# Optimization experiments

Hardware: AMD Instinct MI355X
Metric: run time of the kernel (lower is better)

## Reference

```python
import jax, jax.numpy as jnp
import numpy as np

B, N, K = 4, 1500, 30
NODE_F, EDGE_F, H = 1024, 128, 128
L, NUM_RBF, NUM_POS, NHEADS = 4, 16, 16, 4
DH = H // NHEADS
LN_EPS = 1e-6


def setup_inputs() -> dict:
    key = jax.random.key(0)
    ks = jax.random.split(key, 16)
    g = lambda k, shp: jax.random.normal(k, shp, jnp.float32) / np.sqrt(shp[-2] if len(shp) > 1 else 1.0)
    return {
        'X': jax.random.normal(ks[0], (B, N, 3), jnp.float32) * 10.0,
        'V': jax.random.normal(ks[1], (B, N, NODE_F), jnp.float32),
        'mask': jnp.ones((B, N), jnp.float32),
        'W_v': g(ks[2], (NODE_F, H)), 'b_v': jnp.zeros((H,), jnp.float32),
        'W_e': g(ks[3], (EDGE_F, H)), 'b_e': jnp.zeros((H,), jnp.float32),
        'W_edge': g(ks[4], (NUM_POS + NUM_RBF, EDGE_F)),
        'ln_e_g': jnp.ones((EDGE_F,), jnp.float32), 'ln_e_b': jnp.zeros((EDGE_F,), jnp.float32),
        'Wq': g(ks[5], (L, H, H)), 'Wk': g(ks[6], (L, 2 * H, H)),
        'Wv_a': g(ks[7], (L, 2 * H, H)), 'Wo': g(ks[8], (L, H, H)),
        'ln1_g': jnp.ones((L, H), jnp.float32), 'ln1_b': jnp.zeros((L, H), jnp.float32),
        'ln2_g': jnp.ones((L, H), jnp.float32), 'ln2_b': jnp.zeros((L, H), jnp.float32),
        'W_ff1': g(ks[9], (L, H, 4 * H)), 'b_ff1': jnp.zeros((L, 4 * H), jnp.float32),
        'W_ff2': g(ks[10], (L, 4 * H, H)), 'b_ff2': jnp.zeros((L, H), jnp.float32),
        'W_out': g(ks[11], (H, 1)), 'b_out': jnp.zeros((1,), jnp.float32),
    }


def _layer_norm(x, gamma, beta):
    mu = jnp.mean(x, -1, keepdims=True)
    var = jnp.var(x, -1, keepdims=True)
    return gamma * (x - mu) / jnp.sqrt(var + LN_EPS) + beta


def _gather_nodes(nodes, idx):
    # nodes [B,N,C], idx [B,N,K] -> [B,N,K,C]
    return jax.vmap(lambda n, i: n[i])(nodes, idx)


def reference(X, V, mask, W_v, b_v, W_e, b_e, W_edge, ln_e_g, ln_e_b, Wq, Wk, Wv_a, Wo,
              ln1_g, ln1_b, ln2_g, ln2_b, W_ff1, b_ff1, W_ff2, b_ff2, W_out, b_out):
    # ---- EdgeFeatures: masked pairwise distances + kNN topk ----
    mask2 = mask[:, :, None] * mask[:, None, :]            # [B,N,N]
    dX = X[:, :, None, :] - X[:, None, :, :]               # [B,N,N,3]
    D = mask2 * jnp.sqrt(jnp.sum(dX * dX, -1) + 1e-6)
    D_adj = D + (1.0 - mask2) * jnp.max(D, -1, keepdims=True)
    negD, E_idx = jax.lax.top_k(-D_adj, K)                 # k smallest distances
    D_nb = -negD                                           # [B,N,K]
    # RBF of neighbor distances
    mu = jnp.linspace(0.0, 20.0, NUM_RBF)
    sigma = 20.0 / NUM_RBF
    rbf = jnp.exp(-(((D_nb[..., None] - mu) / sigma) ** 2))  # [B,N,K,NUM_RBF]
    # sinusoidal relative positional encodings of neighbor offsets
    ii = jnp.arange(N, dtype=jnp.float32)[None, :, None]
    d_rel = (E_idx.astype(jnp.float32) - ii)[..., None]
    freq = jnp.exp(jnp.arange(0, NUM_POS, 2, dtype=jnp.float32) * (-np.log(10000.0) / NUM_POS))
    ang = d_rel * freq
    pos = jnp.concatenate([jnp.cos(ang), jnp.sin(ang)], -1)  # [B,N,K,NUM_POS]
    E = jnp.concatenate([pos, rbf], -1) @ W_edge
    E = _layer_norm(E, ln_e_g, ln_e_b)                     # [B,N,K,EDGE_F]
    # ---- node / edge embeddings ----
    h_V = V @ W_v + b_v                                    # [B,N,H]
    h_E = E @ W_e + b_e                                    # [B,N,K,H]
    mask_attend = mask[:, :, None] * _gather_nodes(mask[..., None], E_idx)[..., 0]  # [B,N,K]
    neg_inf = jnp.float32(np.finfo(np.float32).min)
    # ---- encoder layers ----
    for l in range(L):
        h_EV = jnp.concatenate([h_E, _gather_nodes(h_V, E_idx)], -1)  # [B,N,K,2H]
        Q = (h_V @ Wq[l]).reshape(B, N, NHEADS, DH)
        Kh = (h_EV @ Wk[l]).reshape(B, N, K, NHEADS, DH)
        Vh = (h_EV @ Wv_a[l]).reshape(B, N, K, NHEADS, DH)
        logits = jnp.einsum('bnhd,bnkhd->bnhk', Q, Kh) / np.sqrt(DH)
        m = mask_attend[:, :, None, :]                     # [B,N,1,K]
        attend = jax.nn.softmax(jnp.where(m > 0, logits, neg_inf), -1) * m
        upd = jnp.einsum('bnhk,bnkhd->bnhd', attend, Vh).reshape(B, N, H) @ Wo[l]
        h_V = _layer_norm(h_V + upd, ln1_g[l], ln1_b[l])
        dh = jax.nn.relu(h_V @ W_ff1[l] + b_ff1[l]) @ W_ff2[l] + b_ff2[l]
        h_V = _layer_norm(h_V + dh, ln2_g[l], ln2_b[l])
        h_V = mask[..., None] * h_V
    return (h_V @ W_out + b_out)[..., 0]                   # [B,N] logits
```

## Files before the change

### kernel.cpp

```cpp
#include <hip/hip_runtime.h>
#include <hip/hip_bf16.h>
#include <math.h>

#define NB 4
#define NN 1500
#define KNB 30
#define H 128
#define NHEADS 4
#define FFH 512
#define NODE_FEAT 1024
#define NROWS (NB*NN)
#define LN_EPS 1e-6f

#define P_F32_STRIDE 384
#define P_BF16_STRIDE 768

typedef __attribute__((ext_vector_type(8))) short s8v;
typedef __attribute__((ext_vector_type(4))) float f4v;

__device__ __forceinline__ float bf_lo(unsigned u){ union{unsigned i; float f;} v; v.i = u<<16; return v.f; }
__device__ __forceinline__ float bf_hi(unsigned u){ union{unsigned i; float f;} v; v.i = u & 0xffff0000u; return v.f; }

__device__ __forceinline__ void find_bucket30(
    const unsigned* hist, int base0, int t, int lane, int wave,
    int* wsum, int* res)
{
    int h[16], s = 0;
    const uint4* hp = (const uint4*)&hist[(t & 127) * 16];
    int sh = (t >> 7) << 4;
    uint4 w[4] = {hp[0], hp[1], hp[2], hp[3]};
#pragma unroll
    for (int i = 0; i < 4; i++) {
        h[i*4+0] = (w[i].x >> sh) & 0xffff;
        h[i*4+1] = (w[i].y >> sh) & 0xffff;
        h[i*4+2] = (w[i].z >> sh) & 0xffff;
        h[i*4+3] = (w[i].w >> sh) & 0xffff;
        s += h[i*4+0] + h[i*4+1] + h[i*4+2] + h[i*4+3];
    }
    int inc = s;
#pragma unroll
    for (int off = 1; off < 64; off <<= 1) {
        int o = __shfl_up(inc, off, 64);
        if (lane >= off) inc += o;
    }
    if (lane == 63) wsum[wave] = inc;
    __syncthreads();
    int base = base0 + inc - s;
    for (int w2 = 0; w2 < wave; w2++) base += wsum[w2];
    if (base < KNB && base + s >= KNB) {
        int running = base;
#pragma unroll
        for (int i = 0; i < 16; i++) {
            if (running < KNB && running + h[i] >= KNB) { res[0] = (t<<4)|i; res[1] = running; break; }
            running += h[i];
        }
    }
    __syncthreads();
}

__global__ __launch_bounds__(256) void topk_kernel(
    const float* __restrict__ X, const float* __restrict__ mask,
    int* __restrict__ E_idx, float* __restrict__ D_nb)
{
    int row = blockIdx.x;
    int b = row / NN;
    int t = threadIdx.x;
    int wave = t >> 6, lane = t & 63;
    __shared__ float d_adj[NN];
    __shared__ unsigned hist[2048];
    __shared__ float redw[4];
    __shared__ int   wsum[4];
    __shared__ int   res[2];
    __shared__ int   cand[64];
    __shared__ int   ncand;

    float xi0 = X[row*3+0], xi1 = X[row*3+1], xi2 = X[row*3+2];
    float mi = mask[row];

    float dr[6], m2r[6];
    float lmax = -1e30f;
#pragma unroll
    for (int q = 0; q < 6; q++) {
        int j = t + q*256;
        float d = 0.f, m2 = 0.f;
        if (j < NN) {
            float dx = xi0 - X[(b*NN+j)*3+0];
            float dy = xi1 - X[(b*NN+j)*3+1];
            float dz = xi2 - X[(b*NN+j)*3+2];
            d  = sqrtf(dx*dx + dy*dy + dz*dz + 1e-6f);
            m2 = mi * mask[b*NN+j];
            lmax = fmaxf(lmax, m2*d);
        }
        dr[q] = d; m2r[q] = m2;
    }
    for (int q = t; q < 2048; q += 256) hist[q] = 0;
#pragma unroll
    for (int off = 32; off > 0; off >>= 1)
        lmax = fmaxf(lmax, __shfl_xor(lmax, off, 64));
    if (lane == 0) redw[wave] = lmax;
    if (t == 0) ncand = 0;
    __syncthreads();
    float rowmax = fmaxf(fmaxf(redw[0], redw[1]), fmaxf(redw[2], redw[3]));

    unsigned kreg[6];
#pragma unroll
    for (int q = 0; q < 6; q++) {
        int j = t + q*256;
        if (j < NN) {
            float dv = m2r[q]*dr[q] + (1.0f - m2r[q])*rowmax;
            d_adj[j] = dv;
            unsigned key = __float_as_uint(dv);
            kreg[q] = key;
            unsigned bkt = key >> 20;
            atomicAdd(&hist[bkt & 2047], 1u << ((bkt >> 11) << 4));
        } else kreg[q] = 0xFFFFFFFFu;
    }
    __syncthreads();

    find_bucket30(hist, 0, t, lane, wave, wsum, res);
    int B1 = res[0], nb1 = res[1];

    for (int q = t; q < 2048; q += 256) hist[q] = 0;
    __syncthreads();
#pragma unroll
    for (int q = 0; q < 6; q++) {
        if ((kreg[q] >> 20) == (unsigned)B1) {
            unsigned bkt = (kreg[q] >> 8) & 0xFFF;
            atomicAdd(&hist[bkt & 2047], 1u << ((bkt >> 11) << 4));
        }
    }
    __syncthreads();

    find_bucket30(hist, nb1, t, lane, wave, wsum, res);
    unsigned Bfull = ((unsigned)B1 << 12) | (unsigned)res[0];

#pragma unroll
    for (int q = 0; q < 6; q++) {
        if ((kreg[q] >> 8) <= Bfull) {
            int slot = atomicAdd(&ncand, 1);
            if (slot < 64) cand[slot] = t + q*256;
        }
    }
    __syncthreads();

    if (wave == 0) {
        int nc = min(ncand, 64);
        if (lane < nc) {
            int j = cand[lane];
            float v = d_adj[j];
            int rank = 0;
            for (int m = 0; m < nc; m++) {
                int jm = cand[m];
                float vm = d_adj[jm];
                rank += (vm < v || (vm == v && jm < j)) ? 1 : 0;
            }
            if (rank < KNB) {
                E_idx[row*KNB + rank] = j;
                D_nb[row*KNB + rank]  = v;
            }
        }
    }
}

__global__ __launch_bounds__(256) void wprep_edge_kernel(
    const float* __restrict__ W_edge, __hip_bfloat16* __restrict__ W_edge_t)
{
    int tid = blockIdx.x*256 + threadIdx.x;
    int n = tid >> 5, k = tid & 31;
    W_edge_t[tid] = __float2bfloat16(W_edge[k*H + n]);
}

__global__ __launch_bounds__(256) void edge_kernel(
    const int* __restrict__ E_idx, const float* __restrict__ D_nb,
    const __hip_bfloat16* __restrict__ W_edge_t, const float* __restrict__ ln_g,
    const float* __restrict__ ln_b, __hip_bfloat16* __restrict__ E_ln)
{
    int g0 = blockIdx.x * 2;
    int t = threadIdx.x;
    int wave = t >> 6, lane = t & 63, lm = lane & 15, lq = lane >> 4;
    __shared__ __hip_bfloat16 Es[64*136];

    int row = wave*16 + lm;
    int rr = row < 60 ? row : 59;
    int node = g0 + (rr >= KNB ? 1 : 0);
    int e = node*KNB + (rr >= KNB ? rr - KNB : rr);
    float drel = (float)(E_idx[e] - (node % NN));
    float dnb  = D_nb[e];

    const float FR[8] = {1.f, 0.31622776601683794f, 0.1f, 0.031622776601683794f,
                         0.01f, 0.0031622776601683794f, 0.001f, 0.00031622776601683794f};
    union { s8v v; __hip_bfloat16 h[8]; } af;
    if (lq == 0) {
#pragma unroll
        for (int j = 0; j < 8; j++) af.h[j] = __float2bfloat16(cosf(drel*FR[j]));
    } else if (lq == 1) {
#pragma unroll
        for (int j = 0; j < 8; j++) af.h[j] = __float2bfloat16(sinf(drel*FR[j]));
    } else {
        int f0 = (lq-2)*8;
#pragma unroll
        for (int j = 0; j < 8; j++) {
            float mu = (20.0f/15.0f) * (float)(f0+j);
            float z = (dnb - mu) * 0.8f;
            af.h[j] = __float2bfloat16(expf(-z*z));
        }
    }

    f4v acc[8];
#pragma unroll
    for (int nt = 0; nt < 8; nt++) {
        s8v bf = *(const s8v*)&W_edge_t[(nt*16+lm)*32 + lq*8];
        f4v z = {0.f,0.f,0.f,0.f};
        acc[nt] = __builtin_amdgcn_mfma_f32_16x16x32_bf16(af.v, bf, z, 0,0,0);
    }

    float gv[8], bv[8];
#pragma unroll
    for (int nt = 0; nt < 8; nt++) { gv[nt] = ln_g[nt*16+lm]; bv[nt] = ln_b[nt*16+lm]; }
#pragma unroll
    for (int r = 0; r < 4; r++) {
        float sm = 0.f, sq = 0.f;
#pragma unroll
        for (int nt = 0; nt < 8; nt++) { float x = acc[nt][r]; sm += x; sq += x*x; }
#pragma unroll
        for (int m = 1; m < 16; m <<= 1) {
            sm += __shfl_xor(sm, m, 64);
            sq += __shfl_xor(sq, m, 64);
        }
        float mu = sm * (1.0f/H);
        float rs = rsqrtf(sq*(1.0f/H) - mu*mu + LN_EPS);
        int erow = wave*16 + lq*4 + r;
#pragma unroll
        for (int nt = 0; nt < 8; nt++)
            Es[erow*136 + nt*16 + lm] =
                __float2bfloat16(gv[nt]*(acc[nt][r]-mu)*rs + bv[nt]);
    }
    __syncthreads();

    __hip_bfloat16* dst = E_ln + (size_t)g0*KNB*H;
    for (int q = t; q < 960; q += 256) {
        int r = q >> 4, c8 = (q & 15) * 8;
        *(s8v*)&dst[r*H + c8] = *(const s8v*)&Es[r*136 + c8];
    }
}

__global__ __launch_bounds__(256) void wprep_v_kernel(
    const float* __restrict__ W_v, __hip_bfloat16* __restrict__ Wv_t)
{
    int tid = blockIdx.x*256 + threadIdx.x;
    int n = tid & 127, k = tid >> 7;
    Wv_t[(size_t)n*NODE_FEAT + k] = __float2bfloat16(W_v[k*H + n]);
}

__global__ __launch_bounds__(128) void wprep_kv_kernel(
    const float* __restrict__ W_e, const float* __restrict__ b_e,
    const float* __restrict__ Wk, const float* __restrict__ Wv,
    float* __restrict__ Wkv_f, float* __restrict__ bias_kv)
{
    int l = blockIdx.x >> 8;
    int n = blockIdx.x & 255;
    int t = threadIdx.x;
    int col = n & 127;
    const float* W = (n < 128) ? (Wk + l*2*H*H) : (Wv + l*2*H*H);
    __shared__ float wcol[128];
    wcol[t] = W[t*H + col];
    __syncthreads();
    float a = 0.f;
    for (int c = 0; c < H; c += 4) {
        float4 we = *(const float4*)&W_e[t*H + c];
        a += we.x*wcol[c] + we.y*wcol[c+1] + we.z*wcol[c+2] + we.w*wcol[c+3];
    }
    Wkv_f[(size_t)(l*256 + n)*H + t] = a;
    if (t == 0) {
        float bsum = 0.f;
        for (int c = 0; c < H; c++) bsum += b_e[c]*wcol[c];
        bias_kv[l*256 + n] = bsum;
    }
}

__global__ __launch_bounds__(128) void wprep_qp_kernel(
    const float* __restrict__ Wq, const float* __restrict__ Wkv_f,
    __hip_bfloat16* __restrict__ Wn_t)
{
    int l = blockIdx.x >> 9;
    int m = blockIdx.x & 511;
    int h = m >> 7, e = m & 127;
    int c = threadIdx.x;
    __shared__ float wek[32];
    if (c < 32) wek[c] = Wkv_f[(size_t)(l*256 + h*32 + c)*H + e];
    __syncthreads();
    const float* wq = Wq + (size_t)l*16384 + c*128 + h*32;
    float a = 0.f;
#pragma unroll
    for (int d = 0; d < 32; d++) a += wq[d]*wek[d];
    Wn_t[(size_t)(l*896 + 128 + m)*H + c] = __float2bfloat16(a);
}

__global__ __launch_bounds__(128) void wprep_op_kernel(
    const float* __restrict__ Wo, const float* __restrict__ Wkv_f,
    __hip_bfloat16* __restrict__ WoU_t)
{
    int l = blockIdx.x / 640;
    int kk = blockIdx.x - l*640;
    int n = threadIdx.x;
    __shared__ float wev[32];
    if (kk < 512) {
        int h = kk >> 7;
        int e = kk & 127;
        if (n < 32) wev[n] = Wkv_f[(size_t)(l*256 + 128 + h*32 + n)*H + e];
    }
    __syncthreads();
    float v;
    if (kk < 512) {
        int h = kk >> 7;
        float a = 0.f;
#pragma unroll
        for (int d = 0; d < 32; d++)
            a += wev[d]*Wo[(size_t)l*16384 + (h*32+d)*128 + n];
        v = a;
    } else {
        v = Wo[(size_t)l*16384 + (kk-512)*128 + n];
    }
    WoU_t[((size_t)l*128 + n)*640 + kk] = __float2bfloat16(v);
}

__global__ __launch_bounds__(256) void wprep_post_kernel(
    const float* __restrict__ Wf1, const float* __restrict__ Wf2,
    const float* __restrict__ Wq, const float* __restrict__ Wk,
    const float* __restrict__ Wv,
    __hip_bfloat16* __restrict__ Wf1_t, __hip_bfloat16* __restrict__ Wf2_t,
    __hip_bfloat16* __restrict__ Wn_t)
{
    int id = blockIdx.x*256 + threadIdx.x;
    int l = id / 180224;
    int r = id - l*180224;
    float v; __hip_bfloat16* dst;
    if (r < 65536) {
        int n = r >> 7, k = r & 127;
        v = Wf1[(size_t)l*65536 + k*512 + n];
        dst = Wf1_t + (size_t)l*65536 + r;
    } else if (r < 131072) {
        int rr = r - 65536;
        int n = rr >> 9, k = rr & 511;
        v = Wf2[(size_t)l*65536 + k*128 + n];
        dst = Wf2_t + (size_t)l*65536 + rr;
    } else if (r < 147456) {
        int rr = r - 131072;
        int n = rr >> 7, k = rr & 127;
        v = Wq[(size_t)l*16384 + k*128 + n];
        dst = Wn_t + (size_t)l*114688 + rr;
    } else {
        int rr = r - 147456;
        int n = rr >> 7, k = rr & 127;
        v = (n < 128) ? Wk[(size_t)l*32768 + (128+k)*128 + n]
                      : Wv[(size_t)l*32768 + (128+k)*128 + (n-128)];
        dst = Wn_t + (size_t)l*114688 + 81920 + rr;
    }
    *dst = __float2bfloat16(v);
}

__global__ __launch_bounds__(256) void hv_init_kernel(
    const float* __restrict__ V, const __hip_bfloat16* __restrict__ Wv_t,
    const float* __restrict__ b_v, float* __restrict__ hv,
    const __hip_bfloat16* __restrict__ Wn_t, float* __restrict__ P,
    __hip_bfloat16* __restrict__ PKV)
{
    int row0 = blockIdx.x * 16;
    int t = threadIdx.x;
    int wave = t >> 6, lane = t & 63, lm = lane & 15, lq = lane >> 4;
    __shared__ __hip_bfloat16 Vs[16*1032];
    __shared__ __hip_bfloat16 zs[16*136];

    for (int q = t; q < 4096; q += 256) {
        int r = q >> 8, c4 = (q & 255) * 4;
        float4 v4 = *(const float4*)&V[(size_t)(row0+r)*NODE_FEAT + c4];
        __hip_bfloat16* d = &Vs[r*1032 + c4];
        d[0] = __float2bfloat16(v4.x);
        d[1] = __float2bfloat16(v4.y);
        d[2] = __float2bfloat16(v4.z);
        d[3] = __float2bfloat16(v4.w);
    }
    __syncthreads();

#pragma unroll
    for (int ntl = 0; ntl < 2; ntl++) {
        int nt = wave*2 + ntl;
        f4v acc = {0.f,0.f,0.f,0.f};
        for (int ks = 0; ks < 32; ks++) {
            s8v af = *(const s8v*)&Vs[lm*1032 + ks*32 + lq*8];
            s8v bf = *(const s8v*)&Wv_t[(size_t)(nt*16+lm)*NODE_FEAT + ks*32 + lq*8];
            acc = __builtin_amdgcn_mfma_f32_16x16x32_bf16(af, bf, acc, 0,0,0);
        }
        int cc = nt*16 + lm;
        float b = b_v[cc];
#pragma unroll
        for (int r = 0; r < 4; r++) {
            int rr = lq*4 + r;
            float v = acc[r] + b;
            hv[(size_t)(row0+rr)*H + cc] = v;
            zs[rr*136+cc] = __float2bfloat16(v);
        }
    }
    __syncthreads();

    __hip_bfloat16* Pb = (__hip_bfloat16*)P;
    for (int ntl = 0; ntl < 14; ntl++) {
        int nt = wave*14 + ntl;
        f4v acc = {0.f,0.f,0.f,0.f};
#pragma unroll
        for (int ks = 0; ks < 4; ks++) {
            s8v af = *(const s8v*)&zs[lm*136 + ks*32 + lq*8];
            s8v bf = *(const s8v*)&Wn_t[(size_t)(nt*16+lm)*H + ks*32 + lq*8];
            acc = __builtin_amdgcn_mfma_f32_16x16x32_bf16(af, bf, acc, 0,0,0);
        }
        int cc = nt*16 + lm;
#pragma unroll
        for (int r = 0; r < 4; r++) {
            int rr = row0 + lq*4 + r;
            if (cc < 128)
                P[(size_t)rr*P_F32_STRIDE + cc] = acc[r];
            else if (cc < 640)
                Pb[(size_t)rr*P_BF16_STRIDE + 128 + cc] = __float2bfloat16(acc[r]);
            else
                PKV[(size_t)rr*256 + (cc-640)] = __float2bfloat16(acc[r]);
        }
    }
}

__global__ __launch_bounds__(256) void attn_kernel(
    const __hip_bfloat16* __restrict__ E_ln, const float* __restrict__ biasv,
    float* __restrict__ P, const __hip_bfloat16* __restrict__ PKV,
    const int* __restrict__ E_idx, const float* __restrict__ mask)
{
    int g0 = blockIdx.x * 2;
    int t = threadIdx.x;
    int wave = t >> 6, lane = t & 63, lm = lane & 15, lq = lane >> 4;
    __shared__ __hip_bfloat16 Es[60*136];
    __shared__ float Qs[2*128];
    __shared__ __hip_bfloat16 Qp[2*512];
    __shared__ float att_s[2*128];
    __shared__ float ssum[8];
    __shared__ float mv_s[60];
    __shared__ int   nbr[60];

    const __hip_bfloat16* hebase = E_ln + (size_t)g0*KNB*H;
    for (int q = t; q < 960; q += 256) {
        int r = q >> 4, c8 = (q & 15) * 8;
        *(s8v*)&Es[r*136 + c8] = *(const s8v*)&hebase[r*H + c8];
    }
    const __hip_bfloat16* Pb = (const __hip_bfloat16*)P;
    if (t < 128) {
        int node = t >> 6, c8 = (t & 63)*8;
        *(s8v*)&Qp[node*512 + c8] = *(const s8v*)&Pb[(size_t)(g0+node)*P_BF16_STRIDE + 256 + c8];
    }
    {
        int node = t >> 7, c = t & 127;
        Qs[t] = P[(size_t)(g0+node)*P_F32_STRIDE + c];
    }
    if (t < 60) {
        int gn = g0 + t/30;
        int b = gn / NN;
        int idx = E_idx[gn*KNB + (t%30)];
        nbr[t]  = b*NN + idx;
        mv_s[t] = mask[gn] * mask[b*NN + idx];
    }
    __syncthreads();

    if (t < 240) {
        int node = t/120, tt = t%120, h = tt/30, kk = tt%30;
        const uint4* ep = (const uint4*)&Es[(node*30+kk)*136];
        const uint4* qp = (const uint4*)&Qp[node*512 + h*128];
        float a = 0.f;
#pragma unroll
        for (int j = 0; j < 16; j++) {
            uint4 e4 = ep[j], q4 = qp[j];
            a += bf_lo(e4.x)*bf_lo(q4.x) + bf_hi(e4.x)*bf_hi(q4.x);
            a += bf_lo(e4.y)*bf_lo(q4.y) + bf_hi(e4.y)*bf_hi(q4.y);
            a += bf_lo(e4.z)*bf_lo(q4.z) + bf_hi(e4.z)*bf_hi(q4.z);
            a += bf_lo(e4.w)*bf_lo(q4.w) + bf_hi(e4.w)*bf_hi(q4.w);
        }
        const uint4* kb = (const uint4*)(PKV + (size_t)nbr[node*30+kk]*256 + h*32);
        const float* q = &Qs[node*128 + h*32];
#pragma unroll
        for (int j = 0; j < 4; j++) {
            uint4 u = kb[j];
            const float* q8 = q + j*8;
            a += q8[0]*bf_lo(u.x) + q8[1]*bf_hi(u.x)
               + q8[2]*bf_lo(u.y) + q8[3]*bf_hi(u.y)
               + q8[4]*bf_lo(u.z) + q8[5]*bf_hi(u.z)
               + q8[6]*bf_lo(u.w) + q8[7]*bf_hi(u.w);
        }
        int r = node*30 + kk;
        att_s[node*128 + h*32 + kk] =
            (mv_s[r] > 0.f) ? a*0.17677669529663687f : -3.4028235e38f;
    }
    __syncthreads();

    if (wave < 2) {
        int node = wave, h = lq, j = lm;
        float* ap = &att_s[node*128 + h*32];
        const float* mp = &mv_s[node*30];
        float a0 = ap[j];
        float a1 = (j+16 < KNB) ? ap[j+16] : -3.4028235e38f;
        float mx = fmaxf(a0, a1);
#pragma unroll
        for (int m = 1; m < 16; m <<= 1) mx = fmaxf(mx, __shfl_xor(mx, m, 64));
        float e0 = __expf(a0 - mx);
        float e1 = (j+16 < KNB) ? __expf(a1 - mx) : 0.f;
        float s = e0 + e1;
#pragma unroll
        for (int m = 1; m < 16; m <<= 1) s += __shfl_xor(s, m, 64);
        float inv = 1.0f / s;
        float w0 = e0 * inv * mp[j];
        float w1 = (j+16 < KNB) ? e1 * inv * mp[j+16] : 0.f;
        ap[j] = w0;
        if (j+16 < KNB) ap[j+16] = w1;
        float ss = w0 + w1;
#pragma unroll
        for (int m = 1; m < 16; m <<= 1) ss += __shfl_xor(ss, m, 64);
        if (j == 0) ssum[node*4 + h] = ss;
    }
    __syncthreads();

    {
        int node = t >> 7, c = t & 127, h = c >> 5;
        __hip_bfloat16* Ub = (__hip_bfloat16*)P + (size_t)(g0+node)*P_BF16_STRIDE;
        const float* ap = &att_s[node*128];
        const int* nb = &nbr[node*30];

        float u = ssum[node*4 + h] * biasv[c];
        const float* ah = ap + h*32;
        for (int k = 0; k < KNB; k++)
            u += ah[k] * __bfloat162float(PKV[(size_t)nb[k]*256 + 128 + c]);
        Ub[512 + c] = __float2bfloat16(u);

        float s0 = 0.f, s1 = 0.f, s2 = 0.f, s3 = 0.f;
        for (int k = 0; k < KNB; k++) {
            float e = __bfloat162float(Es[(node*30+k)*136 + c]);
            s0 += ap[k]      * e;
            s1 += ap[32+k]   * e;
            s2 += ap[64+k]   * e;
            s3 += ap[96+k]   * e;
        }
        Ub[c]       = __float2bfloat16(s0);
        Ub[128 + c] = __float2bfloat16(s1);
        Ub[256 + c] = __float2bfloat16(s2);
        Ub[384 + c] = __float2bfloat16(s3);
    }
}

__global__ __launch_bounds__(512) void post_kernel(
    float* __restrict__ hv, float* __restrict__ P,
    __hip_bfloat16* __restrict__ PKV, const float* __restrict__ mask,
    const __hip_bfloat16* __restrict__ WoU_t,
    const float* __restrict__ ln1g, const float* __restrict__ ln1b,
    const float* __restrict__ ln2g, const float* __restrict__ ln2b,
    const __hip_bfloat16* __restrict__ Wf1_t, const float* __restrict__ bf1,
    const __hip_bfloat16* __restrict__ Wf2_t, const float* __restrict__ bf2,
    const __hip_bfloat16* __restrict__ Wn_t)
{
    int row0 = blockIdx.x * 16;
    int t = threadIdx.x;
    int wave = t >> 6, lane = t & 63, lm = lane & 15, lq = lane >> 4;

    __shared__ __hip_bfloat16 Aus[16*648];
    __shared__ float xs[16*132];
    __shared__ __hip_bfloat16 ys[16*136];
    __shared__ __hip_bfloat16 t1[16*520];
    __shared__ __hip_bfloat16 zs[16*136];
    __shared__ float ps[512], pq[512];
    __shared__ float mu_s[16], rs_s[16];

    const __hip_bfloat16* Pbc = (const __hip_bfloat16*)P;
    for (int q = t; q < 1280; q += 512) {
        int r = q/80, c8 = (q%80)*8;
        *(s8v*)&Aus[r*648 + c8] = *(const s8v*)&Pbc[(size_t)(row0+r)*P_BF16_STRIDE + c8];
    }
    __syncthreads();

    {
        int nt = wave;
        f4v acc = {0.f,0.f,0.f,0.f};
        for (int ks = 0; ks < 20; ks++) {
            s8v af = *(const s8v*)&Aus[lm*648 + ks*32 + lq*8];
            s8v bf = *(const s8v*)&WoU_t[(size_t)(nt*16+lm)*640 + ks*32 + lq*8];
            acc = __builtin_amdgcn_mfma_f32_16x16x32_bf16(af, bf, acc, 0,0,0);
        }
        int cc = nt*16 + lm;
#pragma unroll
        for (int r = 0; r < 4; r++) {
            int rr = lq*4 + r;
            xs[rr*132+cc] = hv[(size_t)(row0+rr)*128 + cc] + acc[r];
        }
    }
    __syncthreads();

    {
        int r = t >> 5, s = t & 31;
        float4 a = *(const float4*)&xs[r*132 + s*4];
        ps[t] = a.x+a.y+a.z+a.w;
        pq[t] = a.x*a.x+a.y*a.y+a.z*a.z+a.w*a.w;
    }
    __syncthreads();
    if (t < 16) {
        float sm = 0.f, sq = 0.f;
        for (int s = 0; s < 32; s++) { sm += ps[t*32+s]; sq += pq[t*32+s]; }
        float mu = sm*(1.0f/H);
        mu_s[t] = mu;
        rs_s[t] = rsqrtf(sq*(1.0f/H) - mu*mu + LN_EPS);
    }
    __syncthreads();
    for (int q = t; q < 2048; q += 512) {
        int r = q >> 7, c = q & 127;
        float v = ln1g[c]*(xs[r*132+c]-mu_s[r])*rs_s[r] + ln1b[c];
        xs[r*132+c] = v;
        ys[r*136+c] = __float2bfloat16(v);
    }
    __syncthreads();

    for (int ntl = 0; ntl < 4; ntl++) {
        int nt = wave*4 + ntl;
        f4v acc = {0.f,0.f,0.f,0.f};
#pragma unroll
        for (int ks = 0; ks < 4; ks++) {
            s8v af = *(const s8v*)&ys[lm*136 + ks*32 + lq*8];
            s8v bf = *(const s8v*)&Wf1_t[(size_t)(nt*16+lm)*128 + ks*32 + lq*8];
            acc = __builtin_amdgcn_mfma_f32_16x16x32_bf16(af, bf, acc, 0,0,0);
        }
        int cc = nt*16 + lm;
        float b = bf1[cc];
#pragma unroll
        for (int r = 0; r < 4; r++)
            t1[(lq*4+r)*520 + cc] = __float2bfloat16(fmaxf(acc[r]+b, 0.f));
    }
    __syncthreads();

    {
        int nt = wave;
        f4v acc = {0.f,0.f,0.f,0.f};
#pragma unroll
        for (int ks = 0; ks < 16; ks++) {
            s8v af = *(const s8v*)&t1[lm*520 + ks*32 + lq*8];
            s8v bf = *(const s8v*)&Wf2_t[(size_t)(nt*16+lm)*512 + ks*32 + lq*8];
            acc = __builtin_amdgcn_mfma_f32_16x16x32_bf16(af, bf, acc, 0,0,0);
        }
        int cc = nt*16 + lm;
        float b = bf2[cc];
#pragma unroll
        for (int r = 0; r < 4; r++) {
            int rr = lq*4 + r;
            xs[rr*132+cc] = xs[rr*132+cc] + acc[r] + b;
        }
    }
    __syncthreads();

    {
        int r = t >> 5, s = t & 31;
        float4 a = *(const float4*)&xs[r*132 + s*4];
        ps[t] = a.x+a.y+a.z+a.w;
        pq[t] = a.x*a.x+a.y*a.y+a.z*a.z+a.w*a.w;
    }
    __syncthreads();
    if (t < 16) {
        float sm = 0.f, sq = 0.f;
        for (int s = 0; s < 32; s++) { sm += ps[t*32+s]; sq += pq[t*32+s]; }
        float mu = sm*(1.0f/H);
        mu_s[t] = mu;
        rs_s[t] = rsqrtf(sq*(1.0f/H) - mu*mu + LN_EPS);
    }
    __syncthreads();
    for (int q = t; q < 2048; q += 512) {
        int r = q >> 7, c = q & 127;
        float v = mask[row0+r]*(ln2g[c]*(xs[r*132+c]-mu_s[r])*rs_s[r] + ln2b[c]);
        hv[(size_t)(row0+r)*128 + c] = v;
        zs[r*136+c] = __float2bfloat16(v);
    }
    __syncthreads();

    if (Wn_t) {
        __hip_bfloat16* Pbw = (__hip_bfloat16*)P;
        for (int ntl = 0; ntl < 7; ntl++) {
            int nt = wave*7 + ntl;
            f4v acc = {0.f,0.f,0.f,0.f};
#pragma unroll
            for (int ks = 0; ks < 4; ks++) {
                s8v af = *(const s8v*)&zs[lm*136 + ks*32 + lq*8];
                s8v bf = *(const s8v*)&Wn_t[(size_t)(nt*16+lm)*128 + ks*32 + lq*8];
                acc = __builtin_amdgcn_mfma_f32_16x16x32_bf16(af, bf, acc, 0,0,0);
            }
            int cc = nt*16 + lm;
#pragma unroll
            for (int r = 0; r < 4; r++) {
                int rr = row0 + lq*4 + r;
                if (cc < 128)
                    P[(size_t)rr*P_F32_STRIDE + cc] = acc[r];
                else if (cc < 640)
                    Pbw[(size_t)rr*P_BF16_STRIDE + 128 + cc] = __float2bfloat16(acc[r]);
                else
                    PKV[(size_t)rr*256 + (cc-640)] = __float2bfloat16(acc[r]);
            }
        }
    }
}

__global__ __launch_bounds__(64) void out_kernel(
    const float* __restrict__ hv, const float* __restrict__ W_out,
    const float* __restrict__ b_out, float* __restrict__ out)
{
    int row = blockIdx.x;
    int t = threadIdx.x;
    float a = hv[row*H+t]*W_out[t] + hv[row*H+t+64]*W_out[t+64];
#pragma unroll
    for (int s = 32; s > 0; s >>= 1) a += __shfl_down(a, s, 64);
    if (t == 0) out[row] = a + b_out[0];
}

extern "C" void kernel_launch(void* const* d_in, const int* in_sizes, int n_in,
                              void* d_out, int out_size, void* d_ws, size_t ws_size,
                              hipStream_t stream)
{
    const float* X      = (const float*)d_in[0];
    const float* V      = (const float*)d_in[1];
    const float* mask   = (const float*)d_in[2];
    const float* W_v    = (const float*)d_in[3];
    const float* b_v    = (const float*)d_in[4];
    const float* W_e    = (const float*)d_in[5];
    const float* b_e    = (const float*)d_in[6];
    const float* W_edge = (const float*)d_in[7];
    const float* ln_e_g = (const float*)d_in[8];
    const float* ln_e_b = (const float*)d_in[9];
    const float* Wq     = (const float*)d_in[10];
    const float* Wk     = (const float*)d_in[11];
    const float* Wv_a   = (const float*)d_in[12];
    const float* Wo     = (const float*)d_in[13];
    const float* ln1g   = (const float*)d_in[14];
    const float* ln1b   = (const float*)d_in[15];
    const float* ln2g   = (const float*)d_in[16];
    const float* ln2b   = (const float*)d_in[17];
    const float* Wf1    = (const float*)d_in[18];
    const float* bf1    = (const float*)d_in[19];
    const float* Wf2    = (const float*)d_in[20];
    const float* bf2    = (const float*)d_in[21];
    const float* W_out  = (const float*)d_in[22];
    const float* b_out  = (const float*)d_in[23];
    float* out = (float*)d_out;

    char* ws = (char*)d_ws;
    int*            E_idx    = (int*)ws;
    float*          D_nb     = (float*)(ws + 720000);
    __hip_bfloat16* E_ln     = (__hip_bfloat16*)(ws + 1440000);
    float*          hv       = (float*)(ws + 47520000);
    float*          bias_kv  = (float*)(ws + 50592000);
    float*          Wkv_f    = (float*)(ws + 50596096);
    __hip_bfloat16* Wn_t     = (__hip_bfloat16*)(ws + 51120384);
    __hip_bfloat16* WoU_t    = (__hip_bfloat16*)(ws + 52037888);
    __hip_bfloat16* Wf1_t    = (__hip_bfloat16*)(ws + 52693248);
    __hip_bfloat16* Wf2_t    = (__hip_bfloat16*)(ws + 53217536);
    __hip_bfloat16* Wv_t     = (__hip_bfloat16*)(ws + 53741824);
    __hip_bfloat16* W_edge_t = (__hip_bfloat16*)(ws + 54003968);
    __hip_bfloat16* PKV      = (__hip_bfloat16*)(ws + 54012160);
    float*          P        = (float*)(ws + 57084160);

    topk_kernel<<<NROWS, 256, 0, stream>>>(X, mask, E_idx, D_nb);
    wprep_edge_kernel<<<16, 256, 0, stream>>>(W_edge, W_edge_t);
    edge_kernel<<<NROWS/2, 256, 0, stream>>>(E_idx, D_nb, W_edge_t, ln_e_g, ln_e_b, E_ln);
    wprep_kv_kernel<<<1024, 128, 0, stream>>>(W_e, b_e, Wk, Wv_a, Wkv_f, bias_kv);
    wprep_qp_kernel<<<2048, 128, 0, stream>>>(Wq, Wkv_f, Wn_t);
    wprep_op_kernel<<<2560, 128, 0, stream>>>(Wo, Wkv_f, WoU_t);
    wprep_post_kernel<<<2816, 256, 0, stream>>>(Wf1, Wf2, Wq, Wk, Wv_a,
                                                Wf1_t, Wf2_t, Wn_t);
    wprep_v_kernel<<<512, 256, 0, stream>>>(W_v, Wv_t);
    hv_init_kernel<<<NROWS/16, 256, 0, stream>>>(V, Wv_t, b_v, hv, Wn_t, P, PKV);

    for (int l = 0; l < 4; l++) {
        attn_kernel<<<NROWS/2, 256, 0, stream>>>(
            E_ln, bias_kv + l*256 + 128, P, PKV, E_idx, mask);
        post_kernel<<<NROWS/16, 512, 0, stream>>>(
            hv, P, PKV, mask, WoU_t + (size_t)l*81920,
            ln1g + l*H, ln1b + l*H, ln2g + l*H, ln2b + l*H,
            Wf1_t + (size_t)l*65536, bf1 + l*FFH,
            Wf2_t + (size_t)l*65536, bf2 + l*H,
            (l < 3) ? (Wn_t + (size_t)(l+1)*114688) : (const __hip_bfloat16*)nullptr);
    }
    out_kernel<<<NROWS, 64, 0, stream>>>(hv, W_out, b_out, out);
}
```

Baseline: 486.8 us.

## Process 32 rows per post_kernel block to reuse weight fragments across two M-tiles

The post-attention kernel now handles 32 rows per block instead of 16. Each weight fragment loaded from global memory feeds two MFMA tiles, which halves weight traffic per row. LayerNorm is recomputed with per-wave shuffle reductions instead of shared-memory partial sums and extra barriers. Shared buffers are aliased (Aus/t1, ys/zs) to fit the doubled tile. The grid drops to 188 blocks with boundary clamps on the tail, so fewer blocks are available to occupy the CUs.

```diff
diff --git a/kernel.cpp b/kernel.cpp
--- a/kernel.cpp
+++ b/kernel.cpp
@@ -559,121 +559,134 @@
     const __hip_bfloat16* __restrict__ Wf2_t, const float* __restrict__ bf2,
     const __hip_bfloat16* __restrict__ Wn_t)
 {
-    int row0 = blockIdx.x * 16;
+    int row0 = blockIdx.x * 32;
     int t = threadIdx.x;
     int wave = t >> 6, lane = t & 63, lm = lane & 15, lq = lane >> 4;
 
-    __shared__ __hip_bfloat16 Aus[16*648];
-    __shared__ float xs[16*132];
-    __shared__ __hip_bfloat16 ys[16*136];
-    __shared__ __hip_bfloat16 t1[16*520];
-    __shared__ __hip_bfloat16 zs[16*136];
-    __shared__ float ps[512], pq[512];
-    __shared__ float mu_s[16], rs_s[16];
+    __shared__ __hip_bfloat16 AusT1[32*648];
+    __shared__ float xs[32*132];
+    __shared__ __hip_bfloat16 yz[32*136];
+    __hip_bfloat16* Aus = AusT1;
+    __hip_bfloat16* t1  = AusT1;
 
     const __hip_bfloat16* Pbc = (const __hip_bfloat16*)P;
-    for (int q = t; q < 1280; q += 512) {
+    for (int q = t; q < 2560; q += 512) {
         int r = q/80, c8 = (q%80)*8;
-        *(s8v*)&Aus[r*648 + c8] = *(const s8v*)&Pbc[(size_t)(row0+r)*P_BF16_STRIDE + c8];
+        int gr = row0 + r; if (gr > NROWS-1) gr = NROWS-1;
+        *(s8v*)&Aus[r*648 + c8] = *(const s8v*)&Pbc[(size_t)gr*P_BF16_STRIDE + c8];
     }
     __syncthreads();
 
     {
-        int nt = wave;
-        f4v acc = {0.f,0.f,0.f,0.f};
+        int cc = wave*16 + lm;
+        f4v a0 = {0.f,0.f,0.f,0.f}, a1 = a0;
         for (int ks = 0; ks < 20; ks++) {
-            s8v af = *(const s8v*)&Aus[lm*648 + ks*32 + lq*8];
-            s8v bf = *(const s8v*)&WoU_t[(size_t)(nt*16+lm)*640 + ks*32 + lq*8];
-            acc = __builtin_amdgcn_mfma_f32_16x16x32_bf16(af, bf, acc, 0,0,0);
-        }
-        int cc = nt*16 + lm;
+            s8v wf = *(const s8v*)&WoU_t[(size_t)(wave*16+lm)*640 + ks*32 + lq*8];
+            s8v f0 = *(const s8v*)&Aus[lm*648 + ks*32 + lq*8];
+            s8v f1 = *(const s8v*)&Aus[(16+lm)*648 + ks*32 + lq*8];
+            a0 = __builtin_amdgcn_mfma_f32_16x16x32_bf16(f0, wf, a0, 0,0,0);
+            a1 = __builtin_amdgcn_mfma_f32_16x16x32_bf16(f1, wf, a1, 0,0,0);
+        }
 #pragma unroll
         for (int r = 0; r < 4; r++) {
-            int rr = lq*4 + r;
-            xs[rr*132+cc] = hv[(size_t)(row0+rr)*128 + cc] + acc[r];
+            int rr0 = lq*4 + r, rr1 = 16 + lq*4 + r;
+            int g0 = row0 + rr0; if (g0 > NROWS-1) g0 = NROWS-1;
+            int g1 = row0 + rr1; if (g1 > NROWS-1) g1 = NROWS-1;
+            xs[rr0*132+cc] = hv[(size_t)g0*128 + cc] + a0[r];
+            xs[rr1*132+cc] = hv[(size_t)g1*128 + cc] + a1[r];
         }
     }
     __syncthreads();
 
     {
-        int r = t >> 5, s = t & 31;
-        float4 a = *(const float4*)&xs[r*132 + s*4];
-        ps[t] = a.x+a.y+a.z+a.w;
-        pq[t] = a.x*a.x+a.y*a.y+a.z*a.z+a.w*a.w;
-    }
-    __syncthreads();
-    if (t < 16) {
-        float sm = 0.f, sq = 0.f;
-        for (int s = 0; s < 32; s++) { sm += ps[t*32+s]; sq += pq[t*32+s]; }
-        float mu = sm*(1.0f/H);
-        mu_s[t] = mu;
-        rs_s[t] = rsqrtf(sq*(1.0f/H) - mu*mu + LN_EPS);
-    }
-    __syncthreads();
-    for (int q = t; q < 2048; q += 512) {
-        int r = q >> 7, c = q & 127;
-        float v = ln1g[c]*(xs[r*132+c]-mu_s[r])*rs_s[r] + ln1b[c];
-        xs[r*132+c] = v;
-        ys[r*136+c] = __float2bfloat16(v);
+        float g0 = ln1g[lane], g1 = ln1g[64+lane];
+        float b0 = ln1b[lane], b1 = ln1b[64+lane];
+#pragma unroll
+        for (int i = 0; i < 4; i++) {
+            int r = wave*4 + i;
+            float x0 = xs[r*132 + lane], x1 = xs[r*132 + 64 + lane];
+            float sm = x0 + x1, sq = x0*x0 + x1*x1;
+#pragma unroll
+            for (int m = 1; m < 64; m <<= 1) {
+                sm += __shfl_xor(sm, m, 64);
+                sq += __shfl_xor(sq, m, 64);
+            }
+            float mu = sm*(1.0f/H);
+            float rs = rsqrtf(sq*(1.0f/H) - mu*mu + LN_EPS);
+            float v0 = g0*(x0-mu)*rs + b0, v1 = g1*(x1-mu)*rs + b1;
+            xs[r*132 + lane] = v0; xs[r*132 + 64 + lane] = v1;
+            yz[r*136 + lane] = __float2bfloat16(v0);
+            yz[r*136 + 64 + lane] = __float2bfloat16(v1);
+        }
     }
     __syncthreads();
 
     for (int ntl = 0; ntl < 4; ntl++) {
         int nt = wave*4 + ntl;
-        f4v acc = {0.f,0.f,0.f,0.f};
-#pragma unroll
-        for (int ks = 0; ks < 4; ks++) {
-            s8v af = *(const s8v*)&ys[lm*136 + ks*32 + lq*8];
-            s8v bf = *(const s8v*)&Wf1_t[(size_t)(nt*16+lm)*128 + ks*32 + lq*8];
-            acc = __builtin_amdgcn_mfma_f32_16x16x32_bf16(af, bf, acc, 0,0,0);
-        }
         int cc = nt*16 + lm;
         float b = bf1[cc];
-#pragma unroll
-        for (int r = 0; r < 4; r++)
-            t1[(lq*4+r)*520 + cc] = __float2bfloat16(fmaxf(acc[r]+b, 0.f));
+        f4v a0 = {0.f,0.f,0.f,0.f}, a1 = a0;
+#pragma unroll
+        for (int ks = 0; ks < 4; ks++) {
+            s8v wf = *(const s8v*)&Wf1_t[(size_t)(nt*16+lm)*128 + ks*32 + lq*8];
+            s8v f0 = *(const s8v*)&yz[lm*136 + ks*32 + lq*8];
+            s8v f1 = *(const s8v*)&yz[(16+lm)*136 + ks*32 + lq*8];
+            a0 = __builtin_amdgcn_mfma_f32_16x16x32_bf16(f0, wf, a0, 0,0,0);
+            a1 = __builtin_amdgcn_mfma_f32_16x16x32_bf16(f1, wf, a1, 0,0,0);
+        }
+#pragma unroll
+        for (int r = 0; r < 4; r++) {
+            t1[(lq*4+r)*520 + cc]      = __float2bfloat16(fmaxf(a0[r]+b, 0.f));
+            t1[(16+lq*4+r)*520 + cc]   = __float2bfloat16(fmaxf(a1[r]+b, 0.f));
+        }
     }
     __syncthreads();
 
     {
-        int nt = wave;
-        f4v acc = {0.f,0.f,0.f,0.f};
-#pragma unroll
+        int cc = wave*16 + lm;
+        float b = bf2[cc];
+        f4v a0 = {0.f,0.f,0.f,0.f}, a1 = a0;
         for (int ks = 0; ks < 16; ks++) {
-            s8v af = *(const s8v*)&t1[lm*520 + ks*32 + lq*8];
-            s8v bf = *(const s8v*)&Wf2_t[(size_t)(nt*16+lm)*512 + ks*32 + lq*8];
-            acc = __builtin_amdgcn_mfma_f32_16x16x32_bf16(af, bf, acc, 0,0,0);
-        }
-        int cc = nt*16 + lm;
-        float b = bf2[cc];
+            s8v wf = *(const s8v*)&Wf2_t[(size_t)(wave*16+lm)*512 + ks*32 + lq*8];
+            s8v f0 = *(const s8v*)&t1[lm*520 + ks*32 + lq*8];
+            s8v f1 = *(const s8v*)&t1[(16+lm)*520 + ks*32 + lq*8];
+            a0 = __builtin_amdgcn_mfma_f32_16x16x32_bf16(f0, wf, a0, 0,0,0);
+            a1 = __builtin_amdgcn_mfma_f32_16x16x32_bf16(f1, wf, a1, 0,0,0);
+        }
 #pragma unroll
         for (int r = 0; r < 4; r++) {
-            int rr = lq*4 + r;
-            xs[rr*132+cc] = xs[rr*132+cc] + acc[r] + b;
+            int rr0 = lq*4 + r, rr1 = 16 + lq*4 + r;
+            xs[rr0*132+cc] = xs[rr0*132+cc] + a0[r] + b;
+            xs[rr1*132+cc] = xs[rr1*132+cc] + a1[r] + b;
         }
     }
     __syncthreads();
 
     {
-        int r = t >> 5, s = t & 31;
-        float4 a = *(const float4*)&xs[r*132 + s*4];
-        ps[t] = a.x+a.y+a.z+a.w;
-        pq[t] = a.x*a.x+a.y*a.y+a.z*a.z+a.w*a.w;
-    }
-    __syncthreads();
-    if (t < 16) {
-        float sm = 0.f, sq = 0.f;
-        for (int s = 0; s < 32; s++) { sm += ps[t*32+s]; sq += pq[t*32+s]; }
-        float mu = sm*(1.0f/H);
-        mu_s[t] = mu;
-        rs_s[t] = rsqrtf(sq*(1.0f/H) - mu*mu + LN_EPS);
-    }
-    __syncthreads();
-    for (int q = t; q < 2048; q += 512) {
-        int r = q >> 7, c = q & 127;
-        float v = mask[row0+r]*(ln2g[c]*(xs[r*132+c]-mu_s[r])*rs_s[r] + ln2b[c]);
-        hv[(size_t)(row0+r)*128 + c] = v;
-        zs[r*136+c] = __float2bfloat16(v);
+        float g0 = ln2g[lane], g1 = ln2g[64+lane];
+        float b0 = ln2b[lane], b1 = ln2b[64+lane];
+#pragma unroll
+        for (int i = 0; i < 4; i++) {
+            int r = wave*4 + i;
+            int gr = row0 + r;
+            float mk = mask[gr > NROWS-1 ? NROWS-1 : gr];
+            float x0 = xs[r*132 + lane], x1 = xs[r*132 + 64 + lane];
+            float sm = x0 + x1, sq = x0*x0 + x1*x1;
+#pragma unroll
+            for (int m = 1; m < 64; m <<= 1) {
+                sm += __shfl_xor(sm, m, 64);
+                sq += __shfl_xor(sq, m, 64);
+            }
+            float mu = sm*(1.0f/H);
+            float rs = rsqrtf(sq*(1.0f/H) - mu*mu + LN_EPS);
+            float v0 = mk*(g0*(x0-mu)*rs + b0), v1 = mk*(g1*(x1-mu)*rs + b1);
+            yz[r*136 + lane] = __float2bfloat16(v0);
+            yz[r*136 + 64 + lane] = __float2bfloat16(v1);
+            if (gr < NROWS) {
+                hv[(size_t)gr*128 + lane] = v0;
+                hv[(size_t)gr*128 + 64 + lane] = v1;
+            }
+        }
     }
     __syncthreads();
 
@@ -681,23 +694,32 @@
         __hip_bfloat16* Pbw = (__hip_bfloat16*)P;
         for (int ntl = 0; ntl < 7; ntl++) {
             int nt = wave*7 + ntl;
-            f4v acc = {0.f,0.f,0.f,0.f};
+            int cc = nt*16 + lm;
+            f4v a0 = {0.f,0.f,0.f,0.f}, a1 = a0;
 #pragma unroll
             for (int ks = 0; ks < 4; ks++) {
-                s8v af = *(const s8v*)&zs[lm*136 + ks*32 + lq*8];
-                s8v bf = *(const s8v*)&Wn_t[(size_t)(nt*16+lm)*128 + ks*32 + lq*8];
-                acc = __builtin_amdgcn_mfma_f32_16x16x32_bf16(af, bf, acc, 0,0,0);
+                s8v wf = *(const s8v*)&Wn_t[(size_t)(nt*16+lm)*128 + ks*32 + lq*8];
+                s8v f0 = *(const s8v*)&yz[lm*136 + ks*32 + lq*8];
+                s8v f1 = *(const s8v*)&yz[(16+lm)*136 + ks*32 + lq*8];
+                a0 = __builtin_amdgcn_mfma_f32_16x16x32_bf16(f0, wf, a0, 0,0,0);
+                a1 = __builtin_amdgcn_mfma_f32_16x16x32_bf16(f1, wf, a1, 0,0,0);
             }
-            int cc = nt*16 + lm;
-#pragma unroll
-            for (int r = 0; r < 4; r++) {
-                int rr = row0 + lq*4 + r;
-                if (cc < 128)
-                    P[(size_t)rr*P_F32_STRIDE + cc] = acc[r];
-                else if (cc < 640)
-                    Pbw[(size_t)rr*P_BF16_STRIDE + 128 + cc] = __float2bfloat16(acc[r]);
-                else
-                    PKV[(size_t)rr*256 + (cc-640)] = __float2bfloat16(acc[r]);
+#pragma unroll
+            for (int mt = 0; mt < 2; mt++) {
+                f4v* ap = mt ? &a1 : &a0;
+#pragma unroll
+                for (int r = 0; r < 4; r++) {
+                    int rr = row0 + mt*16 + lq*4 + r;
+                    if (rr < NROWS) {
+                        float av = (*ap)[r];
+                        if (cc < 128)
+                            P[(size_t)rr*P_F32_STRIDE + cc] = av;
+                        else if (cc < 640)
+                            Pbw[(size_t)rr*P_BF16_STRIDE + 128 + cc] = __float2bfloat16(av);
+                        else
+                            PKV[(size_t)rr*256 + (cc-640)] = __float2bfloat16(av);
+                    }
+                }
             }
         }
     }
@@ -775,7 +797,7 @@
     for (int l = 0; l < 4; l++) {
         attn_kernel<<<NROWS/2, 256, 0, stream>>>(
             E_ln, bias_kv + l*256 + 128, P, PKV, E_idx, mask);
-        post_kernel<<<NROWS/16, 512, 0, stream>>>(
+        post_kernel<<<(NROWS+31)/32, 512, 0, stream>>>(
             hv, P, PKV, mask, WoU_t + (size_t)l*81920,
             ln1g + l*H, ln1b + l*H, ln2g + l*H, ln2b + l*H,
             Wf1_t + (size_t)l*65536, bf1 + l*FFH,
```

Measured after the change: 438.5 us. -9.9%, faster.
